# Performance work log

Measured on AMD Instinct MI355X. Metric: run time of the kernel, lower is better.

## Reference

```python
import jax, jax.numpy as jnp
import numpy as np

NEG_INF = -9e15  # matches torch's -9000000000000000.0 mask value
LEAKY_SLOPE = 0.2  # init alpha


def setup_inputs() -> dict:
    key = jax.random.key(0)
    k1, k2, k3, k4 = jax.random.split(key, 4)
    N, dim = 4096, 128
    hidden = jax.random.normal(k1, (N, dim), dtype=jnp.float32)
    adj = jax.random.randint(k2, (N, N), 0, 5)  # relation codes 0..4
    W = jax.random.normal(k3, (4, dim), dtype=jnp.float32) * (1.0 / np.sqrt(dim))
    b = jax.random.normal(k4, (4,), dtype=jnp.float32) * 0.01
    return {"hidden": hidden, "adj": adj, "W": W, "b": b}


def reference(hidden, adj, W, b):
    # e_k[i,j] = leakyrelu(sum_d h[i,d]*h[j,d]*W[k,d] + b[k])
    # equivalent to the torch repeat/view outer-product + four dim->1 Linears,
    # computed without materializing the [N,N,dim] intermediate.
    hw = hidden[None, :, :] * W[:, None, :]               # [4, N, dim]
    e = jnp.einsum('knd,md->knm', hw, hidden) + b[:, None, None]  # [4, N, N]
    e = jax.nn.leaky_relu(e, negative_slope=LEAKY_SLOPE)
    neg = jnp.asarray(NEG_INF, dtype=e.dtype)
    alpha = jnp.where(adj == 1, e[0], neg)
    alpha = jnp.where(adj == 2, e[1], alpha)
    alpha = jnp.where(adj == 3, e[2], alpha)
    alpha = jnp.where(adj == 4, e[3], alpha)
    alpha = jax.nn.softmax(alpha, axis=-1)                # [N, N]
    return alpha @ hidden                                  # [N, dim]
```

## Files before the change

### kernel.cpp

```cpp
#include <hip/hip_runtime.h>

#define NN 4096
#define DIM 128
#define TN 64
#define TM 64
#define NSPLIT 8
#define NTILES 8

typedef __attribute__((ext_vector_type(8))) short bf16x8;
typedef __attribute__((ext_vector_type(4))) float f32x4;

#define HRS 136
#define HCS 72
#define HROW_USH (TM * HRS)
#define HCOL_USH (128 * HCS)
#define TILE_USH (HROW_USH + HCOL_USH)
#define TILE_CHUNKS 35
#define PST 72

__device__ inline unsigned short f2bf(float x) {
    union { float f; unsigned u; } v; v.f = x;
    unsigned r = v.u + 0x7FFFu + ((v.u >> 16) & 1u);
    return (unsigned short)(r >> 16);
}

__device__ inline void dma16(const void* g, void* l) {
    __builtin_amdgcn_global_load_lds(
        (const __attribute__((address_space(1))) void*)g,
        (__attribute__((address_space(3))) void*)l,
        16, 0, 0);
}

__global__ __launch_bounds__(256) void prep_pack_kernel(
    const float* __restrict__ hidden,
    unsigned short* __restrict__ Hpack)
{
    __shared__ unsigned short T[16][HCS];
    const int tid = threadIdx.x;
    const int t0  = blockIdx.x >> 3;
    const int s   = blockIdx.x & 7;
    const int m0  = t0 * TM;
    unsigned short* rowdst = Hpack + (size_t)t0 * TILE_USH;
    unsigned short* coldst = rowdst + HROW_USH;

    {
        int row = tid >> 5;
        int c4  = (tid & 31) * 4;
        float4 v = *(const float4*)(hidden + (size_t)(m0 + 8 * s + row) * DIM + c4);
        ushort4 o;
        o.x = f2bf(v.x); o.y = f2bf(v.y); o.z = f2bf(v.z); o.w = f2bf(v.w);
        *(ushort4*)(rowdst + (8 * s + row) * HRS + c4) = o;
    }
    {
        int m  = tid >> 2;
        int dc = (tid & 3) * 4;
        float4 v = *(const float4*)(hidden + (size_t)(m0 + m) * DIM + 16 * s + dc);
        T[dc + 0][m] = f2bf(v.x);
        T[dc + 1][m] = f2bf(v.y);
        T[dc + 2][m] = f2bf(v.z);
        T[dc + 3][m] = f2bf(v.w);
    }
    __syncthreads();
    if (tid < 128) {
        int d  = tid >> 3;
        int c8 = (tid & 7) * 8;
        uint4 v = *(const uint4*)(&T[d][c8]);
        *(uint4*)(coldst + (16 * s + d) * HCS + c8) = v;
    }
}

__global__ __launch_bounds__(256, 2) void gat_flash_kernel(
    const float* __restrict__ hidden,
    const unsigned short* __restrict__ Hpack,
    const int*   __restrict__ adj,
    const float* __restrict__ W,
    const float* __restrict__ bvec,
    float*       __restrict__ Onum,
    float*       __restrict__ lsum)
{
    __shared__ __align__(16) unsigned short HH[2][TILE_USH];
    __shared__ __align__(16) unsigned short Plc[4][16 * PST];

    const int tid  = threadIdx.x;
    const int w    = tid >> 6;
    const int lane = tid & 63;
    const int g    = lane >> 4;
    const int l15  = lane & 15;
    const int blk  = blockIdx.x;
    const int nbr  = blk >> 3;
    const int q8   = blk & 7;
    const int n0   = nbr * TN;
    const int gt0  = q8 * NTILES;
    const int lofs = lane * 16;

    const float b0 = bvec[0], b1 = bvec[1], b2 = bvec[2], b3 = bvec[3];

    {
        const char* src = (const char*)(Hpack + (size_t)gt0 * TILE_USH);
        char* dst = (char*)&HH[0][0];
        #pragma unroll
        for (int it = 0; it < 9; ++it) {
            int chunk = it * 4 + w;
            if (chunk < TILE_CHUNKS)
                dma16(src + chunk * 1024 + lofs, dst + chunk * 1024);
        }
    }

    bf16x8 Af[4][4];
    {
        const int qrow = n0 + w * 16 + l15;
        #pragma unroll
        for (int ks = 0; ks < 4; ++ks) {
            const float* hp = hidden + (size_t)qrow * DIM + ks * 32 + 8 * g;
            float4 h0 = *(const float4*)(hp);
            float4 h1 = *(const float4*)(hp + 4);
            #pragma unroll
            for (int k = 0; k < 4; ++k) {
                const float* wp = W + k * DIM + ks * 32 + 8 * g;
                float4 w0 = *(const float4*)(wp);
                float4 w1 = *(const float4*)(wp + 4);
                bf16x8 a;
                a[0] = (short)f2bf(h0.x * w0.x); a[1] = (short)f2bf(h0.y * w0.y);
                a[2] = (short)f2bf(h0.z * w0.z); a[3] = (short)f2bf(h0.w * w0.w);
                a[4] = (short)f2bf(h1.x * w1.x); a[5] = (short)f2bf(h1.y * w1.y);
                a[6] = (short)f2bf(h1.z * w1.z); a[7] = (short)f2bf(h1.w * w1.w);
                Af[k][ks] = a;
            }
        }
    }

    float plsum = 0.f;
    f32x4 Oacc[8];
    #pragma unroll
    for (int dt = 0; dt < 8; ++dt) Oacc[dt] = (f32x4){0.f, 0.f, 0.f, 0.f};

    const int* arow_ptr = adj + (size_t)(n0 + w * 16 + l15) * NN;
    int4 avc[4], avn[4];
    #pragma unroll
    for (int jt = 0; jt < 4; ++jt)
        avc[jt] = *(const int4*)(arow_ptr + gt0 * TM + jt * 16 + 4 * g);

    __syncthreads();

    unsigned short* Pw = &Plc[w][0];

    for (int tile = 0; tile < NTILES; ++tile) {
        const int cur = tile & 1;
        const int nxt = cur ^ 1;

        if (tile + 1 < NTILES) {
            const char* src = (const char*)(Hpack + (size_t)(gt0 + tile + 1) * TILE_USH);
            char* dst = (char*)&HH[nxt][0];
            #pragma unroll
            for (int it = 0; it < 9; ++it) {
                int chunk = it * 4 + w;
                if (chunk < TILE_CHUNKS)
                    dma16(src + chunk * 1024 + lofs, dst + chunk * 1024);
            }
        }

        #pragma unroll
        for (int jt = 0; jt < 4; ++jt) {
            f32x4 S[4];
            #pragma unroll
            for (int k = 0; k < 4; ++k) S[k] = (f32x4){0.f, 0.f, 0.f, 0.f};
            #pragma unroll
            for (int ks = 0; ks < 4; ++ks) {
                bf16x8 Hf = *(const bf16x8*)&HH[cur][(jt * 16 + l15) * HRS + ks * 32 + 8 * g];
                #pragma unroll
                for (int k = 0; k < 4; ++k)
                    S[k] = __builtin_amdgcn_mfma_f32_16x16x32_bf16(Hf, Af[k][ks], S[k], 0, 0, 0);
            }
            const int4 av = avc[jt];
            float p[4];
            #pragma unroll
            for (int t = 0; t < 4; ++t) {
                const int a = (t == 0) ? av.x : (t == 1) ? av.y : (t == 2) ? av.z : av.w;
                float s = S[0][t] + b0;
                s = (a == 2) ? S[1][t] + b1 : s;
                s = (a == 3) ? S[2][t] + b2 : s;
                s = (a == 4) ? S[3][t] + b3 : s;
                float e = fmaxf(s, 0.2f * s);
                float pp = __expf(e);
                pp = (a == 0) ? 0.f : pp;
                plsum += pp;
                p[t] = pp;
            }
            unsigned r01, r23;
            asm("v_cvt_pk_bf16_f32 %0, %1, %2" : "=v"(r01) : "v"(p[0]), "v"(p[1]));
            asm("v_cvt_pk_bf16_f32 %0, %1, %2" : "=v"(r23) : "v"(p[2]), "v"(p[3]));
            uint2 r2; r2.x = r01; r2.y = r23;
            *(uint2*)(Pw + l15 * PST + jt * 16 + 4 * g) = r2;
        }

        if (tile + 1 < NTILES) {
            #pragma unroll
            for (int jt = 0; jt < 4; ++jt)
                avn[jt] = *(const int4*)(arow_ptr + (gt0 + tile + 1) * TM + jt * 16 + 4 * g);
        }

        #pragma unroll
        for (int kc = 0; kc < 2; ++kc) {
            bf16x8 Pa = *(const bf16x8*)&Pw[l15 * PST + kc * 32 + 8 * g];
            #pragma unroll
            for (int dt = 0; dt < 8; ++dt) {
                bf16x8 Bv = *(const bf16x8*)&HH[cur][HROW_USH + (dt * 16 + l15) * HCS + kc * 32 + 8 * g];
                Oacc[dt] = __builtin_amdgcn_mfma_f32_16x16x32_bf16(Pa, Bv, Oacc[dt], 0, 0, 0);
            }
        }

        #pragma unroll
        for (int i = 0; i < 4; ++i) avc[i] = avn[i];
        __syncthreads();
    }

    {
        float v = plsum;
        v += __shfl_xor(v, 16);
        v += __shfl_xor(v, 32);
        if (lane < 16) atomicAdd(&lsum[n0 + w * 16 + l15], v);
    }
    const int orow0 = n0 + w * 16 + 4 * g;
    #pragma unroll
    for (int dt = 0; dt < 8; ++dt)
        #pragma unroll
        for (int t = 0; t < 4; ++t)
            atomicAdd(&Onum[(size_t)(orow0 + t) * DIM + dt * 16 + l15], Oacc[dt][t]);
}

__global__ __launch_bounds__(256) void combine_kernel(
    const float* __restrict__ Onum, const float* __restrict__ lsum,
    float* __restrict__ out)
{
    int idx = blockIdx.x * 256 + threadIdx.x;
    out[idx] = Onum[idx] / lsum[idx >> 7];
}

extern "C" void kernel_launch(void* const* d_in, const int* in_sizes, int n_in,
                              void* d_out, int out_size, void* d_ws, size_t ws_size,
                              hipStream_t stream) {
    const float* hidden = (const float*)d_in[0];
    const int*   adj    = (const int*)d_in[1];
    const float* W      = (const float*)d_in[2];
    const float* b      = (const float*)d_in[3];
    float* out = (float*)d_out;

    char* ws = (char*)d_ws;
    unsigned short* Hpack = (unsigned short*)ws;
    float* Onum = (float*)(ws + (4u << 20));
    float* lsum = (float*)(ws + (6u << 20));
    hipMemsetAsync(ws + (4u << 20), 0, (2u << 20) + NN * sizeof(float), stream);

    prep_pack_kernel<<<(NN / TM) * 8, 256, 0, stream>>>(hidden, Hpack);
    gat_flash_kernel<<<(NN / TN) * NSPLIT, 256, 0, stream>>>(hidden, Hpack, adj, W, b, Onum, lsum);
    combine_kernel<<<NN * DIM / 256, 256, 0, stream>>>(Onum, lsum, out);
}
```

Before: 130.3 us.

## Permute key rows so P stays in registers as MFMA operand, dropping LDS round-trip

The prep kernel now stores the row-major H tile with a permuted row order, so the QK^T MFMA output layout matches the A-operand layout needed by the PV MFMA. The probability fragments are packed straight into registers instead of being written to and read back from per-wave LDS. This removes LDS stores and loads and the Plc buffer, which frees shared memory. The adjacency loads are remapped to the permuted column order to keep results correct.

```diff
diff --git a/kernel.cpp b/kernel.cpp
--- a/kernel.cpp
+++ b/kernel.cpp
@@ -9,6 +9,7 @@
 
 typedef __attribute__((ext_vector_type(8))) short bf16x8;
 typedef __attribute__((ext_vector_type(4))) float f32x4;
+typedef __attribute__((ext_vector_type(4))) unsigned u32x4;
 
 #define HRS 136
 #define HCS 72
@@ -16,7 +17,6 @@
 #define HCOL_USH (128 * HCS)
 #define TILE_USH (HROW_USH + HCOL_USH)
 #define TILE_CHUNKS 35
-#define PST 72
 
 __device__ inline unsigned short f2bf(float x) {
     union { float f; unsigned u; } v; v.f = x;
@@ -46,10 +46,13 @@
     {
         int row = tid >> 5;
         int c4  = (tid & 31) * 4;
-        float4 v = *(const float4*)(hidden + (size_t)(m0 + 8 * s + row) * DIM + c4);
+        int j   = 8 * s + row;
+        int pj  = ((j >> 2) & 1) * 32 + ((j >> 5) & 1) * 16
+                + ((j >> 3) & 3) * 4  + (j & 3);
+        float4 v = *(const float4*)(hidden + (size_t)(m0 + j) * DIM + c4);
         ushort4 o;
         o.x = f2bf(v.x); o.y = f2bf(v.y); o.z = f2bf(v.z); o.w = f2bf(v.w);
-        *(ushort4*)(rowdst + (8 * s + row) * HRS + c4) = o;
+        *(ushort4*)(rowdst + pj * HRS + c4) = o;
     }
     {
         int m  = tid >> 2;
@@ -79,7 +82,6 @@
     float*       __restrict__ lsum)
 {
     __shared__ __align__(16) unsigned short HH[2][TILE_USH];
-    __shared__ __align__(16) unsigned short Plc[4][16 * PST];
 
     const int tid  = threadIdx.x;
     const int w    = tid >> 6;
@@ -135,14 +137,17 @@
     for (int dt = 0; dt < 8; ++dt) Oacc[dt] = (f32x4){0.f, 0.f, 0.f, 0.f};
 
     const int* arow_ptr = adj + (size_t)(n0 + w * 16 + l15) * NN;
+    const int joff0 = 8 * g;
+    const int joff1 = 32 + 8 * g;
+    const int joff2 = 8 * g + 4;
+    const int joff3 = 32 + 8 * g + 4;
     int4 avc[4], avn[4];
-    #pragma unroll
-    for (int jt = 0; jt < 4; ++jt)
-        avc[jt] = *(const int4*)(arow_ptr + gt0 * TM + jt * 16 + 4 * g);
+    avc[0] = *(const int4*)(arow_ptr + gt0 * TM + joff0);
+    avc[1] = *(const int4*)(arow_ptr + gt0 * TM + joff1);
+    avc[2] = *(const int4*)(arow_ptr + gt0 * TM + joff2);
+    avc[3] = *(const int4*)(arow_ptr + gt0 * TM + joff3);
 
     __syncthreads();
-
-    unsigned short* Pw = &Plc[w][0];
 
     for (int tile = 0; tile < NTILES; ++tile) {
         const int cur = tile & 1;
@@ -159,53 +164,67 @@
             }
         }
 
-        #pragma unroll
-        for (int jt = 0; jt < 4; ++jt) {
-            f32x4 S[4];
-            #pragma unroll
-            for (int k = 0; k < 4; ++k) S[k] = (f32x4){0.f, 0.f, 0.f, 0.f};
-            #pragma unroll
-            for (int ks = 0; ks < 4; ++ks) {
-                bf16x8 Hf = *(const bf16x8*)&HH[cur][(jt * 16 + l15) * HRS + ks * 32 + 8 * g];
-                #pragma unroll
-                for (int k = 0; k < 4; ++k)
-                    S[k] = __builtin_amdgcn_mfma_f32_16x16x32_bf16(Hf, Af[k][ks], S[k], 0, 0, 0);
-            }
-            const int4 av = avc[jt];
-            float p[4];
-            #pragma unroll
-            for (int t = 0; t < 4; ++t) {
-                const int a = (t == 0) ? av.x : (t == 1) ? av.y : (t == 2) ? av.z : av.w;
-                float s = S[0][t] + b0;
-                s = (a == 2) ? S[1][t] + b1 : s;
-                s = (a == 3) ? S[2][t] + b2 : s;
-                s = (a == 4) ? S[3][t] + b3 : s;
-                float e = fmaxf(s, 0.2f * s);
-                float pp = __expf(e);
-                pp = (a == 0) ? 0.f : pp;
-                plsum += pp;
-                p[t] = pp;
-            }
-            unsigned r01, r23;
-            asm("v_cvt_pk_bf16_f32 %0, %1, %2" : "=v"(r01) : "v"(p[0]), "v"(p[1]));
-            asm("v_cvt_pk_bf16_f32 %0, %1, %2" : "=v"(r23) : "v"(p[2]), "v"(p[3]));
-            uint2 r2; r2.x = r01; r2.y = r23;
-            *(uint2*)(Pw + l15 * PST + jt * 16 + 4 * g) = r2;
-        }
+        u32x4 paw0, paw1;
+
+#define QK_SLICE(S, W0, W1)                                                        \
+        {                                                                          \
+            f32x4 Sv[4];                                                           \
+            _Pragma("unroll")                                                      \
+            for (int k = 0; k < 4; ++k) Sv[k] = (f32x4){0.f, 0.f, 0.f, 0.f};       \
+            _Pragma("unroll")                                                      \
+            for (int ks = 0; ks < 4; ++ks) {                                       \
+                bf16x8 Hf = *(const bf16x8*)&HH[cur][((S) * 16 + l15) * HRS + ks * 32 + 8 * g]; \
+                _Pragma("unroll")                                                  \
+                for (int k = 0; k < 4; ++k)                                        \
+                    Sv[k] = __builtin_amdgcn_mfma_f32_16x16x32_bf16(Hf, Af[k][ks], Sv[k], 0, 0, 0); \
+            }                                                                      \
+            const int4 av = avc[S];                                                \
+            float p[4];                                                            \
+            _Pragma("unroll")                                                      \
+            for (int t = 0; t < 4; ++t) {                                          \
+                const int a = (t == 0) ? av.x : (t == 1) ? av.y : (t == 2) ? av.z : av.w; \
+                float sc = Sv[0][t] + b0;                                          \
+                sc = (a == 2) ? Sv[1][t] + b1 : sc;                                \
+                sc = (a == 3) ? Sv[2][t] + b2 : sc;                                \
+                sc = (a == 4) ? Sv[3][t] + b3 : sc;                                \
+                float e = fmaxf(sc, 0.2f * sc);                                    \
+                float pp = __expf(e);                 \
+                pp = (a == 0) ? 0.f : pp;                                          \
+                plsum += pp;                                                       \
+                p[t] = pp;                                                         \
+            }                                                                      \
+            unsigned r01, r23;                                                     \
+            asm("v_cvt_pk_bf16_f32 %0, %1, %2" : "=v"(r01) : "v"(p[0]), "v"(p[1])); \
+            asm("v_cvt_pk_bf16_f32 %0, %1, %2" : "=v"(r23) : "v"(p[2]), "v"(p[3])); \
+            W0 = r01; W1 = r23;                                                    \
+        }
+
+        QK_SLICE(0, paw0.x, paw0.y)
+        QK_SLICE(1, paw1.x, paw1.y)
+        QK_SLICE(2, paw0.z, paw0.w)
+        QK_SLICE(3, paw1.z, paw1.w)
+#undef QK_SLICE
 
         if (tile + 1 < NTILES) {
-            #pragma unroll
-            for (int jt = 0; jt < 4; ++jt)
-                avn[jt] = *(const int4*)(arow_ptr + (gt0 + tile + 1) * TM + jt * 16 + 4 * g);
-        }
-
-        #pragma unroll
-        for (int kc = 0; kc < 2; ++kc) {
-            bf16x8 Pa = *(const bf16x8*)&Pw[l15 * PST + kc * 32 + 8 * g];
+            const int* ap = arow_ptr + (gt0 + tile + 1) * TM;
+            avn[0] = *(const int4*)(ap + joff0);
+            avn[1] = *(const int4*)(ap + joff1);
+            avn[2] = *(const int4*)(ap + joff2);
+            avn[3] = *(const int4*)(ap + joff3);
+        }
+
+        {
+            bf16x8 Pa0 = __builtin_bit_cast(bf16x8, paw0);
+            bf16x8 Pa1 = __builtin_bit_cast(bf16x8, paw1);
             #pragma unroll
             for (int dt = 0; dt < 8; ++dt) {
-                bf16x8 Bv = *(const bf16x8*)&HH[cur][HROW_USH + (dt * 16 + l15) * HCS + kc * 32 + 8 * g];
-                Oacc[dt] = __builtin_amdgcn_mfma_f32_16x16x32_bf16(Pa, Bv, Oacc[dt], 0, 0, 0);
+                bf16x8 Bv0 = *(const bf16x8*)&HH[cur][HROW_USH + (dt * 16 + l15) * HCS + 8 * g];
+                Oacc[dt] = __builtin_amdgcn_mfma_f32_16x16x32_bf16(Pa0, Bv0, Oacc[dt], 0, 0, 0);
+            }
+            #pragma unroll
+            for (int dt = 0; dt < 8; ++dt) {
+                bf16x8 Bv1 = *(const bf16x8*)&HH[cur][HROW_USH + (dt * 16 + l15) * HCS + 32 + 8 * g];
+                Oacc[dt] = __builtin_amdgcn_mfma_f32_16x16x32_bf16(Pa1, Bv1, Oacc[dt], 0, 0, 0);
             }
         }
 
```

Result: no change. 128.6 us (-1.3%).
